# Performance work log

Measured on AMD Instinct MI355X. Metric: run time of the kernel, lower is better.

Reference implementation:

```python
import jax, jax.numpy as jnp
import numpy as np

B, MODEL_DIM, HIGH_DIM, T, KEEP = 8, 1024, 2048, 4096, 64


def setup_inputs() -> dict:
    key = jax.random.key(0)
    k1, k2, k3, k4, k5 = jax.random.split(key, 5)
    x = jax.random.normal(k1, (B, MODEL_DIM, T), dtype=jnp.float32)
    # conv1d kernel-size-1 weights == dense matrices; torch default uniform init
    s_e = 1.0 / np.sqrt(MODEL_DIM)
    W_e = jax.random.uniform(k2, (HIGH_DIM, MODEL_DIM), jnp.float32, -s_e, s_e)
    b_e = jax.random.uniform(k3, (HIGH_DIM,), jnp.float32, -s_e, s_e)
    s_c = 1.0 / np.sqrt(HIGH_DIM)
    W_c = jax.random.uniform(k4, (MODEL_DIM, HIGH_DIM), jnp.float32, -s_c, s_c)
    b_c = jax.random.uniform(k5, (MODEL_DIM,), jnp.float32, -s_c, s_c)
    return {"x": x, "W_e": W_e, "b_e": b_e, "W_c": W_c, "b_c": b_c}


def reference(x, W_e, b_e, W_c, b_c):
    # expand: 1x1 conv == per-timestep GEMM  [B,C,T] -> [B,D,T]
    y = jnp.einsum('bct,dc->bdt', x, W_e) + b_e[None, :, None]
    # top-k along time axis per (batch, channel) row; keep only those entries
    vals, idx = jax.lax.top_k(y, KEEP)            # [B,D,KEEP]
    sparse = jnp.zeros_like(y).at[
        jnp.arange(B)[:, None, None],
        jnp.arange(HIGH_DIM)[None, :, None],
        idx,
    ].set(vals)                                   # [B,D,T] sparse activation
    # contract: 1x1 conv back to model_dim
    out = jnp.einsum('bdt,md->bmt', sparse, W_c) + b_c[None, :, None]
    return (out, sparse)
```

## Files before the change

kernel.cpp:

```cpp
#include <hip/hip_runtime.h>
#include <hip/hip_bf16.h>
#include <stdint.h>

#define B_    8
#define MD    1024
#define HD    2048
#define T_    4096
#define KEEP_ 64
#define CAP   96
#define BANDW 4e-3f
#define AMB   2e-6
#define NCAND 512

typedef __attribute__((ext_vector_type(8))) short short8;
typedef __attribute__((ext_vector_type(4))) float f32x4;
typedef __attribute__((ext_vector_type(8))) _Float16 half8;

__device__ __forceinline__ void gload_lds16(const void* g, void* l) {
    __builtin_amdgcn_global_load_lds(
        (const __attribute__((address_space(1))) uint32_t*)g,
        (__attribute__((address_space(3))) uint32_t*)l, 16, 0, 0);
}

__device__ __forceinline__ short f2h(float a) {
    _Float16 h = (_Float16)a;
    short s;
    __builtin_memcpy(&s, &h, 2);
    return s;
}

__device__ __forceinline__ float h2f(short s) {
    _Float16 h;
    __builtin_memcpy(&h, &s, 2);
    return (float)h;
}

__device__ __forceinline__ void split1h(float a, short& h, short& l) {
    _Float16 hh = (_Float16)a;
    float r = a - (float)hh;
    h = f2h(a);
    l = f2h(r);
    (void)hh;
}

__device__ __forceinline__ uint32_t sortable(float f) {
    uint32_t u = __float_as_uint(f);
    return (u & 0x80000000u) ? ~u : (u | 0x80000000u);
}

__global__ void k_transpose_wc(const float* __restrict__ Wc,
                               __hip_bfloat16* __restrict__ WcT) {
    __shared__ float s[32][33];
    const int d0 = blockIdx.x * 32;
    const int m0 = blockIdx.y * 32;
    const int tx = threadIdx.x;
    const int ty = threadIdx.y;
    #pragma unroll
    for (int k = 0; k < 4; k++)
        s[ty + k * 8][tx] = Wc[(size_t)(m0 + ty + k * 8) * HD + d0 + tx];
    __syncthreads();
    #pragma unroll
    for (int k = 0; k < 4; k++)
        WcT[(size_t)(d0 + ty + k * 8) * MD + m0 + tx] =
            __float2bfloat16(s[tx][ty + k * 8]);
}

__global__ void k_round_we(const float* __restrict__ We,
                           short* __restrict__ hi) {
    const int i = (blockIdx.x * 256 + threadIdx.x) * 4;
    float4 v = *(const float4*)&We[i];
    short4 h;
    h.x = f2h(v.x);
    h.y = f2h(v.y);
    h.z = f2h(v.z);
    h.w = f2h(v.w);
    *(short4*)&hi[i] = h;
}

__global__ void k_split_x(const float* __restrict__ x,
                          short* __restrict__ xTh, short* __restrict__ xTl) {
    __shared__ float s[32][33];
    const int t0 = blockIdx.x * 32;
    const int c0 = blockIdx.y * 32;
    const int b  = blockIdx.z;
    const int tx = threadIdx.x;
    const int ty = threadIdx.y;
    const float* xb = x + (size_t)b * MD * T_;
    #pragma unroll
    for (int k = 0; k < 4; k++)
        s[ty + k * 8][tx] = xb[(size_t)(c0 + ty + k * 8) * T_ + t0 + tx];
    __syncthreads();
    const int id = ty * 32 + tx;
    const int tl = id >> 3;
    const int c4 = (id & 7) * 4;
    short4 h4, l4;
    split1h(s[c4 + 0][tl], h4.x, l4.x);
    split1h(s[c4 + 1][tl], h4.y, l4.y);
    split1h(s[c4 + 2][tl], h4.z, l4.z);
    split1h(s[c4 + 3][tl], h4.w, l4.w);
    const size_t o = ((size_t)b * T_ + t0 + tl) * MD + c0 + c4;
    *(short4*)&xTh[o] = h4;
    *(short4*)&xTl[o] = l4;
}

__launch_bounds__(256)
__global__ void k_gemm_mfma(const short* __restrict__ xTh,
                            const short* __restrict__ Weh,
                            const float* __restrict__ be,
                            float* __restrict__ y) {
    __shared__ __align__(16) short Ah[128 * 32];
    __shared__ __align__(16) short Bh[128 * 32];

    const int t0  = blockIdx.x * 128;
    const int d0  = blockIdx.y * 128;
    const int b   = blockIdx.z;
    const int tid = threadIdx.x;
    const int lane = tid & 63;
    const int wave = tid >> 6;
    const int wm = wave >> 1, wn = wave & 1;
    const int fm = lane & 15, fq = lane >> 4;

    const short* A_h = Weh + (size_t)d0 * MD;
    const short* B_h = xTh + ((size_t)b * T_ + t0) * MD;

    f32x4 acc[4][4];
    #pragma unroll
    for (int i = 0; i < 4; i++)
        #pragma unroll
        for (int j = 0; j < 4; j++) acc[i][j] = (f32x4)0.f;

    for (int k0 = 0; k0 < MD; k0 += 32) {
        #pragma unroll
        for (int i = 0; i < 2; i++) {
            const int e   = i * 256 + tid;
            const int row = e >> 2, kc = (e & 3) << 3;
            const size_t go = (size_t)row * MD + k0 + kc;
            const int lo = e << 3;
            gload_lds16(A_h + go, &Ah[lo]);
            gload_lds16(B_h + go, &Bh[lo]);
        }
        __syncthreads();

        half8 ah[4], bh[4];
        #pragma unroll
        for (int mt = 0; mt < 4; mt++) {
            const int r = wm * 64 + mt * 16 + fm;
            ah[mt] = *(const half8*)&Ah[r * 32 + fq * 8];
        }
        #pragma unroll
        for (int nt = 0; nt < 4; nt++) {
            const int r = wn * 64 + nt * 16 + fm;
            bh[nt] = *(const half8*)&Bh[r * 32 + fq * 8];
        }
        #pragma unroll
        for (int mt = 0; mt < 4; mt++)
            #pragma unroll
            for (int nt = 0; nt < 4; nt++)
                acc[mt][nt] = __builtin_amdgcn_mfma_f32_16x16x32_f16(
                    ah[mt], bh[nt], acc[mt][nt], 0, 0, 0);
        __syncthreads();
    }

    float* yb = y + (size_t)b * HD * T_;
    #pragma unroll
    for (int mt = 0; mt < 4; mt++) {
        #pragma unroll
        for (int r = 0; r < 4; r++) {
            const int d = d0 + wm * 64 + mt * 16 + fq * 4 + r;
            const float bias = be[d];
            float* yd = yb + (size_t)d * T_ + t0 + wn * 64 + fm;
            #pragma unroll
            for (int nt = 0; nt < 4; nt++)
                yd[nt * 16] = acc[mt][nt][r] + bias;
        }
    }
}

__launch_bounds__(256)
__global__ void k_topk(float* __restrict__ y,
                       const float* __restrict__ x,
                       const float* __restrict__ We,
                       const float* __restrict__ be,
                       const short* __restrict__ xTh,
                       const short* __restrict__ xTl,
                       int* __restrict__ colcnt, float2* __restrict__ collist) {
    __shared__ double s_redd[256];
    __shared__ float  s_fred[8];
    __shared__ int    s_ired[8];
    __shared__ uint32_t s_cu[NCAND];
    __shared__ int      s_ci[NCAND];
    __shared__ int s_n;
    __shared__ uint32_t s_Vu;
    __shared__ int s_bidx[64];
    __shared__ double s_bval[64];
    __shared__ unsigned char s_bkeep[64];
    __shared__ int s_nhi, s_nb, s_flag;

    const int row  = blockIdx.x;
    const int b    = row >> 11;
    const int d    = row & 2047;
    const int tid  = threadIdx.x;
    const int lane = tid & 63;
    const int wave = tid >> 6;
    float* yrow = y + (size_t)row * T_;

    float4 fv[4];
    #pragma unroll
    for (int j = 0; j < 4; j++)
        fv[j] = *(const float4*)&yrow[(j * 256 + tid) * 4];

    float s1 = 0.f, s2 = 0.f;
    #pragma unroll
    for (int j = 0; j < 4; j++) {
        const float* p = (const float*)&fv[j];
        #pragma unroll
        for (int e = 0; e < 4; e++) { s1 += p[e]; s2 = fmaf(p[e], p[e], s2); }
    }
    for (int off = 32; off > 0; off >>= 1) {
        s1 += __shfl_down(s1, off);
        s2 += __shfl_down(s2, off);
    }
    if (lane == 0) { s_fred[wave] = s1; s_fred[4 + wave] = s2; }
    __syncthreads();
    const float S1 = s_fred[0] + s_fred[1] + s_fred[2] + s_fred[3];
    const float S2 = s_fred[4] + s_fred[5] + s_fred[6] + s_fred[7];
    const float mu = S1 * (1.f / T_);
    const float sd = sqrtf(fmaxf(S2 * (1.f / T_) - mu * mu, 1e-20f));

    float thr = mu + 1.8f * sd;
    int total = 0;
    for (int iter = 0; iter < 16; iter++) {
        int c = 0;
        #pragma unroll
        for (int j = 0; j < 4; j++) {
            const float* p = (const float*)&fv[j];
            #pragma unroll
            for (int e = 0; e < 4; e++) c += (p[e] >= thr);
        }
        for (int off = 32; off > 0; off >>= 1) c += __shfl_down(c, off);
        __syncthreads();
        if (lane == 0) s_ired[wave] = c;
        __syncthreads();
        total = s_ired[0] + s_ired[1] + s_ired[2] + s_ired[3];
        if (total >= KEEP_ && total <= NCAND) break;
        thr += (total < KEEP_) ? (-0.3f * sd) : (0.3f * sd);
    }

    if (tid == 0) { s_n = 0; s_Vu = 0; }
    __syncthreads();
    #pragma unroll
    for (int j = 0; j < 4; j++) {
        const float* p = (const float*)&fv[j];
        #pragma unroll
        for (int e = 0; e < 4; e++) {
            if (p[e] >= thr) {
                const int pos = atomicAdd(&s_n, 1);
                if (pos < NCAND) {
                    s_cu[pos] = sortable(p[e]);
                    s_ci[pos] = (j * 256 + tid) * 4 + e;
                }
            }
        }
    }
    __syncthreads();
    int nc = min(s_n, NCAND);

    for (int ci = tid; ci < nc; ci += 256) {
        const uint32_t u = s_cu[ci];
        const int id = s_ci[ci];
        int r = 0;
        for (int j = 0; j < nc; j++) {
            const uint32_t uj = s_cu[j];
            r += (uj > u) || (uj == u && s_ci[j] < id);
        }
        if (r == KEEP_ - 1) s_Vu = u;
    }
    __syncthreads();
    const uint32_t Vu = s_Vu;
    const uint32_t Vb = (Vu & 0x80000000u) ? (Vu & 0x7FFFFFFFu) : ~Vu;
    const float Vf = __uint_as_float(Vb);
    const float hi_thr = Vf + BANDW;
    const float lo_thr = Vf - BANDW;
    const uint32_t hiU = sortable(hi_thr);
    const uint32_t loU = sortable(lo_thr);

    if (lo_thr < thr) {
        __syncthreads();
        if (tid == 0) s_n = 0;
        __syncthreads();
        #pragma unroll
        for (int j = 0; j < 4; j++) {
            const float* p = (const float*)&fv[j];
            #pragma unroll
            for (int e = 0; e < 4; e++) {
                if (p[e] >= lo_thr) {
                    const int pos = atomicAdd(&s_n, 1);
                    if (pos < NCAND) {
                        s_cu[pos] = sortable(p[e]);
                        s_ci[pos] = (j * 256 + tid) * 4 + e;
                    }
                }
            }
        }
        __syncthreads();
        nc = min(s_n, NCAND);
    }

    if (tid == 0) { s_nhi = 0; s_nb = 0; }
    __syncthreads();
    for (int ci = tid; ci < nc; ci += 256) {
        const uint32_t u = s_cu[ci];
        if (u > hiU) {
            atomicAdd(&s_nhi, 1);
        } else if (u >= loU) {
            const int p = atomicAdd(&s_nb, 1);
            if (p < 64) s_bidx[p] = s_ci[ci];
        }
    }
    __syncthreads();
    const int nb    = min(s_nb, 64);
    const int slots = KEEP_ - s_nhi;

    if (nb > slots) {
        const int c0 = tid * 4;
        const float4 w4 = *(const float4*)&We[(size_t)d * MD + c0];
        for (int j = 0; j < nb; j++) {
            const size_t xo = ((size_t)b * T_ + s_bidx[j]) * MD + c0;
            const short4 h4 = *(const short4*)&xTh[xo];
            const short4 l4 = *(const short4*)&xTl[xo];
            const float x0 = h2f(h4.x) + h2f(l4.x);
            const float x1 = h2f(h4.y) + h2f(l4.y);
            const float x2 = h2f(h4.z) + h2f(l4.z);
            const float x3 = h2f(h4.w) + h2f(l4.w);
            double partial = (double)w4.x * (double)x0
                           + (double)w4.y * (double)x1
                           + (double)w4.z * (double)x2
                           + (double)w4.w * (double)x3;
            s_redd[tid] = partial;
            __syncthreads();
            for (int off = 128; off > 0; off >>= 1) {
                if (tid < off) s_redd[tid] += s_redd[tid + off];
                __syncthreads();
            }
            if (tid == 0) s_bval[j] = s_redd[0] + (double)be[d];
            __syncthreads();
        }
        if (tid < nb) {
            const double v = s_bval[tid];
            const int    ti = s_bidx[tid];
            int rank = 0;
            for (int j = 0; j < nb; j++) {
                if (j == tid) continue;
                if (s_bval[j] > v ||
                    (s_bval[j] == v && s_bidx[j] < ti)) rank++;
            }
            s_bkeep[tid] = (rank < slots) ? 1 : 0;
        }
        __syncthreads();
        if (tid == 0) {
            double kmin = 1e300, dmax = -1e300;
            for (int j = 0; j < nb; j++) {
                if (s_bkeep[j]) { if (s_bval[j] < kmin) kmin = s_bval[j]; }
                else            { if (s_bval[j] > dmax) dmax = s_bval[j]; }
            }
            s_flag = (kmin - dmax < AMB) ? 1 : 0;
        }
        __syncthreads();
        if (s_flag) {
            for (int j = 0; j < nb; j++) {
                const int t = s_bidx[j];
                double partial = 0.0;
                for (int c = tid; c < MD; c += 256)
                    partial += (double)We[(size_t)d * MD + c] *
                               (double)x[((size_t)b * MD + c) * T_ + t];
                s_redd[tid] = partial;
                __syncthreads();
                for (int off = 128; off > 0; off >>= 1) {
                    if (tid < off) s_redd[tid] += s_redd[tid + off];
                    __syncthreads();
                }
                if (tid == 0) s_bval[j] = s_redd[0] + (double)be[d];
                __syncthreads();
            }
            if (tid < nb) {
                const double v = s_bval[tid];
                const int    ti = s_bidx[tid];
                int rank = 0;
                for (int j = 0; j < nb; j++) {
                    if (j == tid) continue;
                    if (s_bval[j] > v ||
                        (s_bval[j] == v && s_bidx[j] < ti)) rank++;
                }
                s_bkeep[tid] = (rank < slots) ? 1 : 0;
            }
        }
    } else {
        if (tid < nb) s_bkeep[tid] = 1;
    }
    __syncthreads();

    #pragma unroll
    for (int j = 0; j < 4; j++) {
        float* p = (float*)&fv[j];
        #pragma unroll
        for (int e = 0; e < 4; e++) {
            const int i = (j * 256 + tid) * 4 + e;
            const float f = p[e];
            const uint32_t u = sortable(f);
            bool keep;
            if (u > hiU) {
                keep = true;
            } else if (u < loU) {
                keep = false;
            } else {
                keep = false;
                for (int q = 0; q < nb; q++)
                    if (s_bidx[q] == i) { keep = (s_bkeep[q] != 0); break; }
            }
            if (keep) {
                const int col = b * T_ + i;
                const int pos = atomicAdd(&colcnt[col], 1);
                if (pos < CAP)
                    collist[(size_t)col * CAP + pos] =
                        make_float2(__int_as_float(d), f);
            } else {
                p[e] = 0.0f;
            }
        }
        *(float4*)&yrow[(j * 256 + tid) * 4] = fv[j];
    }
}

__launch_bounds__(256)
__global__ void k_contract(const int* __restrict__ colcnt,
                           const float2* __restrict__ collist,
                           const __hip_bfloat16* __restrict__ WcT,
                           const float* __restrict__ bc,
                           float* __restrict__ out) {
    __shared__ float2 s_list[16][CAP];
    __shared__ int    s_cnt[16];
    __shared__ float  s_t[256][17];

    const int t0  = blockIdx.x * 16;
    const int b   = blockIdx.y;
    const int tid = threadIdx.x;

    if (tid < 16) s_cnt[tid] = min(colcnt[b * T_ + t0 + tid], CAP);
    __syncthreads();
    for (int c = 0; c < 16; c++) {
        const int n = s_cnt[c];
        for (int i = tid; i < n; i += 256)
            s_list[c][i] = collist[(size_t)(b * T_ + t0 + c) * CAP + i];
    }
    __syncthreads();

    for (int mc = 0; mc < 4; mc++) {
        const int m = mc * 256 + tid;
        const float bias = bc[m];
        float acc[16];
        #pragma unroll
        for (int c = 0; c < 16; c++) acc[c] = bias;

        #pragma unroll
        for (int c = 0; c < 16; c++) {
            const int n = s_cnt[c];
            float a = acc[c];
            int i = 0;
            for (; i + 4 <= n; i += 4) {
                const float2 e0 = s_list[c][i + 0];
                const float2 e1 = s_list[c][i + 1];
                const float2 e2 = s_list[c][i + 2];
                const float2 e3 = s_list[c][i + 3];
                const float w0 = __bfloat162float(
                    WcT[(size_t)__float_as_int(e0.x) * MD + m]);
                const float w1 = __bfloat162float(
                    WcT[(size_t)__float_as_int(e1.x) * MD + m]);
                const float w2 = __bfloat162float(
                    WcT[(size_t)__float_as_int(e2.x) * MD + m]);
                const float w3 = __bfloat162float(
                    WcT[(size_t)__float_as_int(e3.x) * MD + m]);
                a = fmaf(e0.y, w0, a);
                a = fmaf(e1.y, w1, a);
                a = fmaf(e2.y, w2, a);
                a = fmaf(e3.y, w3, a);
            }
            for (; i < n; i++) {
                const float2 e = s_list[c][i];
                const float w = __bfloat162float(
                    WcT[(size_t)__float_as_int(e.x) * MD + m]);
                a = fmaf(e.y, w, a);
            }
            acc[c] = a;
        }

        #pragma unroll
        for (int c = 0; c < 16; c++) s_t[tid][c] = acc[c];
        __syncthreads();
        #pragma unroll
        for (int pass = 0; pass < 4; pass++) {
            const int r  = pass * 64 + (tid >> 2);
            const int cj = (tid & 3) * 4;
            float4 v;
            v.x = s_t[r][cj + 0];
            v.y = s_t[r][cj + 1];
            v.z = s_t[r][cj + 2];
            v.w = s_t[r][cj + 3];
            const int m_out = mc * 256 + r;
            *(float4*)&out[((size_t)b * MD + m_out) * T_ + t0 + cj] = v;
        }
        __syncthreads();
    }
}

extern "C" void kernel_launch(void* const* d_in, const int* in_sizes, int n_in,
                              void* d_out, int out_size, void* d_ws, size_t ws_size,
                              hipStream_t stream) {
    const float* x  = (const float*)d_in[0];
    const float* We = (const float*)d_in[1];
    const float* be = (const float*)d_in[2];
    const float* Wc = (const float*)d_in[3];
    const float* bc = (const float*)d_in[4];

    float* out0 = (float*)d_out;
    float* out1 = out0 + (size_t)B_ * MD * T_;

    char* ws = (char*)d_ws;
    int*     colcnt  = (int*)ws;
    float2*  collist = (float2*)(ws + (size_t)B_ * T_ * sizeof(int));
    __hip_bfloat16* WcT =
        (__hip_bfloat16*)(ws + (size_t)B_ * T_ * sizeof(int) +
                          (size_t)B_ * T_ * CAP * sizeof(float2));

    short* xTh = (short*)out0;
    short* xTl = xTh + (size_t)B_ * T_ * MD;
    short* Weh = (short*)collist;

    hipMemsetAsync(colcnt, 0, (size_t)B_ * T_ * sizeof(int), stream);

    k_transpose_wc<<<dim3(HD / 32, MD / 32), dim3(32, 8), 0, stream>>>(Wc, WcT);
    k_round_we<<<(HD * MD) / 1024, 256, 0, stream>>>(We, Weh);
    k_split_x<<<dim3(T_ / 32, MD / 32, B_), dim3(32, 8), 0, stream>>>(x, xTh, xTl);
    k_gemm_mfma<<<dim3(T_ / 128, HD / 128, B_), 256, 0, stream>>>(
        xTh, Weh, be, out1);
    k_topk<<<B_ * HD, 256, 0, stream>>>(out1, x, We, be, xTh, xTl,
                                        colcnt, collist);
    k_contract<<<dim3(T_ / 16, B_), 256, 0, stream>>>(colcnt, collist, WcT, bc, out0);
}
```

Before: 1.212 ms.

## Store expand GEMM output as fp16 in-place, pack top-k keys, wave-parallel band recompute

The expand GEMM now writes fp16 values into the first half of each fp32 output row instead of full fp32, and the top-k kernel reads them back as short8 vectors. This halves the intermediate write and read traffic on the dense activation. Candidate value and index are packed into one 64-bit key so ranking needs one comparison, and the band recompute uses one wave per candidate with shuffle reductions instead of a block-wide shared-memory tree. The fp16 rounding is covered by a slightly wider band and exact fp64 recomputation, but the in-place half-row aliasing depends on each row being read before it is overwritten.

```diff
diff --git a/kernel.cpp b/kernel.cpp
--- a/kernel.cpp
+++ b/kernel.cpp
@@ -8,7 +8,7 @@
 #define T_    4096
 #define KEEP_ 64
 #define CAP   96
-#define BANDW 4e-3f
+#define BANDW 5e-3f
 #define AMB   2e-6
 #define NCAND 512
 
@@ -161,17 +161,18 @@
         __syncthreads();
     }
 
-    float* yb = y + (size_t)b * HD * T_;
+    _Float16* yh = (_Float16*)y;
     #pragma unroll
     for (int mt = 0; mt < 4; mt++) {
         #pragma unroll
         for (int r = 0; r < 4; r++) {
             const int d = d0 + wm * 64 + mt * 16 + fq * 4 + r;
             const float bias = be[d];
-            float* yd = yb + (size_t)d * T_ + t0 + wn * 64 + fm;
+            _Float16* yd = yh + ((size_t)b * HD + d) * (2 * T_)
+                              + t0 + wn * 64 + fm;
             #pragma unroll
             for (int nt = 0; nt < 4; nt++)
-                yd[nt * 16] = acc[mt][nt][r] + bias;
+                yd[nt * 16] = (_Float16)(acc[mt][nt][r] + bias);
         }
     }
 }
@@ -187,8 +188,7 @@
     __shared__ double s_redd[256];
     __shared__ float  s_fred[8];
     __shared__ int    s_ired[8];
-    __shared__ uint32_t s_cu[NCAND];
-    __shared__ int      s_ci[NCAND];
+    __shared__ unsigned long long s_ck[NCAND];
     __shared__ int s_n;
     __shared__ uint32_t s_Vu;
     __shared__ int s_bidx[64];
@@ -204,18 +204,16 @@
     const int wave = tid >> 6;
     float* yrow = y + (size_t)row * T_;
 
-    float4 fv[4];
-    #pragma unroll
-    for (int j = 0; j < 4; j++)
-        fv[j] = *(const float4*)&yrow[(j * 256 + tid) * 4];
+    const short* yrow16 = (const short*)yrow;
+    short8 r0 = *(const short8*)&yrow16[(size_t)tid * 8];
+    short8 r1 = *(const short8*)&yrow16[(size_t)(256 + tid) * 8];
+    float fv[16];
+    #pragma unroll
+    for (int e = 0; e < 8; e++) { fv[e] = h2f(r0[e]); fv[8 + e] = h2f(r1[e]); }
 
     float s1 = 0.f, s2 = 0.f;
     #pragma unroll
-    for (int j = 0; j < 4; j++) {
-        const float* p = (const float*)&fv[j];
-        #pragma unroll
-        for (int e = 0; e < 4; e++) { s1 += p[e]; s2 = fmaf(p[e], p[e], s2); }
-    }
+    for (int q = 0; q < 16; q++) { s1 += fv[q]; s2 = fmaf(fv[q], fv[q], s2); }
     for (int off = 32; off > 0; off >>= 1) {
         s1 += __shfl_down(s1, off);
         s2 += __shfl_down(s2, off);
@@ -227,53 +225,41 @@
     const float mu = S1 * (1.f / T_);
     const float sd = sqrtf(fmaxf(S2 * (1.f / T_) - mu * mu, 1e-20f));
 
-    float thr = mu + 1.8f * sd;
+    float thr = mu + 2.0f * sd;
     int total = 0;
     for (int iter = 0; iter < 16; iter++) {
         int c = 0;
         #pragma unroll
-        for (int j = 0; j < 4; j++) {
-            const float* p = (const float*)&fv[j];
-            #pragma unroll
-            for (int e = 0; e < 4; e++) c += (p[e] >= thr);
-        }
+        for (int q = 0; q < 16; q++) c += (fv[q] >= thr);
         for (int off = 32; off > 0; off >>= 1) c += __shfl_down(c, off);
         __syncthreads();
         if (lane == 0) s_ired[wave] = c;
         __syncthreads();
         total = s_ired[0] + s_ired[1] + s_ired[2] + s_ired[3];
         if (total >= KEEP_ && total <= NCAND) break;
-        thr += (total < KEEP_) ? (-0.3f * sd) : (0.3f * sd);
+        thr += (total < KEEP_) ? (-0.25f * sd) : (0.25f * sd);
     }
 
     if (tid == 0) { s_n = 0; s_Vu = 0; }
     __syncthreads();
     #pragma unroll
-    for (int j = 0; j < 4; j++) {
-        const float* p = (const float*)&fv[j];
-        #pragma unroll
-        for (int e = 0; e < 4; e++) {
-            if (p[e] >= thr) {
-                const int pos = atomicAdd(&s_n, 1);
-                if (pos < NCAND) {
-                    s_cu[pos] = sortable(p[e]);
-                    s_ci[pos] = (j * 256 + tid) * 4 + e;
-                }
-            }
+    for (int q = 0; q < 16; q++) {
+        if (fv[q] >= thr) {
+            const int i = (q < 8) ? (tid * 8 + q) : (2048 + tid * 8 + (q - 8));
+            const int pos = atomicAdd(&s_n, 1);
+            if (pos < NCAND)
+                s_ck[pos] = ((unsigned long long)sortable(fv[q]) << 32) |
+                            (uint32_t)(~i);
         }
     }
     __syncthreads();
     int nc = min(s_n, NCAND);
 
     for (int ci = tid; ci < nc; ci += 256) {
-        const uint32_t u = s_cu[ci];
-        const int id = s_ci[ci];
+        const unsigned long long k = s_ck[ci];
         int r = 0;
-        for (int j = 0; j < nc; j++) {
-            const uint32_t uj = s_cu[j];
-            r += (uj > u) || (uj == u && s_ci[j] < id);
-        }
-        if (r == KEEP_ - 1) s_Vu = u;
+        for (int j = 0; j < nc; j++) r += (s_ck[j] > k);
+        if (r == KEEP_ - 1) s_Vu = (uint32_t)(k >> 32);
     }
     __syncthreads();
     const uint32_t Vu = s_Vu;
@@ -289,17 +275,14 @@
         if (tid == 0) s_n = 0;
         __syncthreads();
         #pragma unroll
-        for (int j = 0; j < 4; j++) {
-            const float* p = (const float*)&fv[j];
-            #pragma unroll
-            for (int e = 0; e < 4; e++) {
-                if (p[e] >= lo_thr) {
-                    const int pos = atomicAdd(&s_n, 1);
-                    if (pos < NCAND) {
-                        s_cu[pos] = sortable(p[e]);
-                        s_ci[pos] = (j * 256 + tid) * 4 + e;
-                    }
-                }
+        for (int q = 0; q < 16; q++) {
+            if (fv[q] >= lo_thr) {
+                const int i = (q < 8) ? (tid * 8 + q)
+                                      : (2048 + tid * 8 + (q - 8));
+                const int pos = atomicAdd(&s_n, 1);
+                if (pos < NCAND)
+                    s_ck[pos] = ((unsigned long long)sortable(fv[q]) << 32) |
+                                (uint32_t)(~i);
             }
         }
         __syncthreads();
@@ -309,12 +292,13 @@
     if (tid == 0) { s_nhi = 0; s_nb = 0; }
     __syncthreads();
     for (int ci = tid; ci < nc; ci += 256) {
-        const uint32_t u = s_cu[ci];
+        const unsigned long long k = s_ck[ci];
+        const uint32_t u = (uint32_t)(k >> 32);
         if (u > hiU) {
             atomicAdd(&s_nhi, 1);
         } else if (u >= loU) {
             const int p = atomicAdd(&s_nb, 1);
-            if (p < 64) s_bidx[p] = s_ci[ci];
+            if (p < 64) s_bidx[p] = (int)(~(uint32_t)k & 0xFFFFu);
         }
     }
     __syncthreads();
@@ -322,29 +306,28 @@
     const int slots = KEEP_ - s_nhi;
 
     if (nb > slots) {
-        const int c0 = tid * 4;
-        const float4 w4 = *(const float4*)&We[(size_t)d * MD + c0];
-        for (int j = 0; j < nb; j++) {
-            const size_t xo = ((size_t)b * T_ + s_bidx[j]) * MD + c0;
-            const short4 h4 = *(const short4*)&xTh[xo];
-            const short4 l4 = *(const short4*)&xTl[xo];
-            const float x0 = h2f(h4.x) + h2f(l4.x);
-            const float x1 = h2f(h4.y) + h2f(l4.y);
-            const float x2 = h2f(h4.z) + h2f(l4.z);
-            const float x3 = h2f(h4.w) + h2f(l4.w);
-            double partial = (double)w4.x * (double)x0
-                           + (double)w4.y * (double)x1
-                           + (double)w4.z * (double)x2
-                           + (double)w4.w * (double)x3;
-            s_redd[tid] = partial;
-            __syncthreads();
-            for (int off = 128; off > 0; off >>= 1) {
-                if (tid < off) s_redd[tid] += s_redd[tid + off];
-                __syncthreads();
-            }
-            if (tid == 0) s_bval[j] = s_redd[0] + (double)be[d];
-            __syncthreads();
-        }
+        const int c0l = lane * 16;
+        const float* wrow = We + (size_t)d * MD;
+        for (int j = wave; j < nb; j += 4) {
+            const int t = s_bidx[j];
+            const size_t xo = ((size_t)b * T_ + t) * MD + c0l;
+            double acc = 0.0;
+            #pragma unroll
+            for (int qq = 0; qq < 4; qq++) {
+                const float4 w4 = *(const float4*)&wrow[c0l + qq * 4];
+                const short4 h4 = *(const short4*)&xTh[xo + qq * 4];
+                const short4 l4 = *(const short4*)&xTl[xo + qq * 4];
+                acc += (double)w4.x * (double)(h2f(h4.x) + h2f(l4.x));
+                acc += (double)w4.y * (double)(h2f(h4.y) + h2f(l4.y));
+                acc += (double)w4.z * (double)(h2f(h4.z) + h2f(l4.z));
+                acc += (double)w4.w * (double)(h2f(h4.w) + h2f(l4.w));
+            }
+            #pragma unroll
+            for (int off = 32; off > 0; off >>= 1)
+                acc += __shfl_down(acc, off);
+            if (lane == 0) s_bval[j] = acc + (double)be[d];
+        }
+        __syncthreads();
         if (tid < nb) {
             const double v = s_bval[tid];
             const int    ti = s_bidx[tid];
@@ -400,12 +383,13 @@
     __syncthreads();
 
     #pragma unroll
-    for (int j = 0; j < 4; j++) {
-        float* p = (float*)&fv[j];
-        #pragma unroll
-        for (int e = 0; e < 4; e++) {
-            const int i = (j * 256 + tid) * 4 + e;
-            const float f = p[e];
+    for (int jj = 0; jj < 2; jj++) {
+        float buf[8];
+        #pragma unroll
+        for (int e = 0; e < 8; e++) {
+            const int q = jj * 8 + e;
+            const int i = jj * 2048 + tid * 8 + e;
+            const float f = fv[q];
             const uint32_t u = sortable(f);
             bool keep;
             if (u > hiU) {
@@ -414,8 +398,8 @@
                 keep = false;
             } else {
                 keep = false;
-                for (int q = 0; q < nb; q++)
-                    if (s_bidx[q] == i) { keep = (s_bkeep[q] != 0); break; }
+                for (int p = 0; p < nb; p++)
+                    if (s_bidx[p] == i) { keep = (s_bkeep[p] != 0); break; }
             }
             if (keep) {
                 const int col = b * T_ + i;
@@ -423,11 +407,14 @@
                 if (pos < CAP)
                     collist[(size_t)col * CAP + pos] =
                         make_float2(__int_as_float(d), f);
+                buf[e] = f;
             } else {
-                p[e] = 0.0f;
-            }
-        }
-        *(float4*)&yrow[(j * 256 + tid) * 4] = fv[j];
+                buf[e] = 0.0f;
+            }
+        }
+        float* base = yrow + jj * 2048 + (size_t)tid * 8;
+        *(float4*)(base)     = make_float4(buf[0], buf[1], buf[2], buf[3]);
+        *(float4*)(base + 4) = make_float4(buf[4], buf[5], buf[6], buf[7]);
     }
 }
 
```

New measurement: 1.167 ms. -3.7%, faster.
